# Performance work log

Measured on AMD Instinct MI355X. Metric: run time of the kernel, lower is better.

Reference implementation:

```python
import jax, jax.numpy as jnp
import numpy as np

F_DIM = 128
H_DIM = 128
T_DIM = H_DIM // 4          # 32
D = H_DIM + T_DIM           # 160, block hidden dim
N_NODES = 100000
N_EDGES = 800000
N_LAYERS = 2
LN_EPS = 1e-5


def _layernorm(x, g, b):
    m = jnp.mean(x, axis=-1, keepdims=True)
    v = jnp.mean(jnp.square(x - m), axis=-1, keepdims=True)
    return (x - m) * jax.lax.rsqrt(v + LN_EPS) * g + b


def setup_inputs() -> dict:
    key = jax.random.key(0)
    ks = jax.random.split(key, 24)
    p = lambda k, shape: jax.random.normal(k, shape, dtype=jnp.float32) * 0.05
    inp = {
        "node_features": jax.random.normal(ks[0], (N_NODES, F_DIM), dtype=jnp.float32),
        "edge_index": jax.random.randint(ks[1], (2, N_EDGES), 0, N_NODES, dtype=jnp.int32),
        "edge_weights": jax.random.uniform(ks[2], (N_EDGES,), dtype=jnp.float32),
        "time_steps": jax.random.uniform(ks[3], (N_NODES, 1), dtype=jnp.float32),
        # node encoder: Linear(F,H) + LN(H)
        "w_enc": p(ks[4], (H_DIM, F_DIM)), "b_enc": jnp.zeros((H_DIM,)),
        "g_enc": jnp.ones((H_DIM,)), "be_enc": jnp.zeros((H_DIM,)),
        # time encoder: Linear(1,T) + LN(T)
        "w_time": p(ks[5], (T_DIM, 1)), "b_time": jnp.zeros((T_DIM,)),
        "g_time": jnp.ones((T_DIM,)), "be_time": jnp.zeros((T_DIM,)),
        # per-layer block params (stacked over layers)
        "wm": p(ks[6], (N_LAYERS, D, 2 * D)), "bm": jnp.zeros((N_LAYERS, D)),
        "gm": jnp.ones((N_LAYERS, D)), "bem": jnp.zeros((N_LAYERS, D)),
        "wu": p(ks[7], (N_LAYERS, D, 2 * D)), "bu": jnp.zeros((N_LAYERS, D)),
        "gu": jnp.ones((N_LAYERS, D)), "beu": jnp.zeros((N_LAYERS, D)),
        "wg": p(ks[8], (N_LAYERS, 1, D)), "bg": jnp.zeros((N_LAYERS, 1)),
        # output projection Linear(D, F)
        "w_out": p(ks[9], (F_DIM, D)), "b_out": jnp.zeros((F_DIM,)),
    }
    return inp


def _block(h, src, dst, w, wm, bm, gm, bem, wu, bu, gu, beu, wg, bg):
    n = h.shape[0]
    # gather endpoints -> per-edge message MLP -> weight -> scatter-add mean
    ecat = jnp.concatenate([h[src], h[dst]], axis=-1)              # [E, 2D]
    em = jax.nn.relu(_layernorm(ecat @ wm.T + bm, gm, bem)) * w[:, None]
    msum = jax.ops.segment_sum(em, dst, num_segments=n)            # [N, D]
    cnt = jax.ops.segment_sum(jnp.ones_like(w), dst, num_segments=n)[:, None]
    valid = (cnt > 0).astype(h.dtype)
    messages = msum / (cnt + 1e-8) * valid
    tw = jax.nn.sigmoid(h @ wg.T + bg)                             # [N, 1]
    h_new = jax.nn.relu(_layernorm(jnp.concatenate([h, messages], axis=-1) @ wu.T + bu, gu, beu))
    return tw * h_new + (1 - tw) * h


def reference(node_features, edge_index, edge_weights, time_steps,
              w_enc, b_enc, g_enc, be_enc, w_time, b_time, g_time, be_time,
              wm, bm, gm, bem, wu, bu, gu, beu, wg, bg, w_out, b_out):
    src, dst = edge_index[0], edge_index[1]
    h = jax.nn.relu(_layernorm(node_features @ w_enc.T + b_enc, g_enc, be_enc))
    t = jax.nn.relu(_layernorm(time_steps @ w_time.T + b_time, g_time, be_time))
    h_t = jnp.concatenate([h, t], axis=-1)                          # [N, D]
    for l in range(N_LAYERS):
        h_t = _block(h_t, src, dst, edge_weights,
                     wm[l], bm[l], gm[l], bem[l],
                     wu[l], bu[l], gu[l], beu[l], wg[l], bg[l])
    out = h_t @ w_out.T + b_out
    # F.normalize(dim=-1), eps=1e-12
    norm = jnp.linalg.norm(out, axis=-1, keepdims=True)
    return out / jnp.maximum(norm, 1e-12)
```

## Files before the change

kernel.cpp:

```cpp
#include <hip/hip_runtime.h>

#define NN 100000
#define NE 800000

typedef _Float16 half8 __attribute__((ext_vector_type(8)));
typedef _Float16 half4 __attribute__((ext_vector_type(4)));
typedef float floatx4 __attribute__((ext_vector_type(4)));

#define LDB(Wf, f) (*(const half8*)&(Wf)[(f) * 512])

__global__ __launch_bounds__(256) void k_zero(float4* __restrict__ p, int n4) {
  int i = blockIdx.x * 256 + threadIdx.x;
  if (i < n4) p[i] = make_float4(0.f, 0.f, 0.f, 0.f);
}

__global__ __launch_bounds__(256) void k_pack(
    const float* __restrict__ w_enc, const float* __restrict__ w_out,
    const float* __restrict__ wu, const float* __restrict__ wm,
    _Float16* __restrict__ WeP, _Float16* __restrict__ WoP,
    _Float16* __restrict__ WuP, _Float16* __restrict__ WpP) {
  int gid = blockIdx.x * 256 + threadIdx.x;
  int fid = gid >> 6, lane = gid & 63;
  int mrow = lane & 15, quad = lane >> 4;
  const float* src; _Float16* dst; int stride, NI, f, g;
  if (fid < 32) {
    f = fid; g = f; src = w_enc; dst = WeP; stride = 128; NI = 8;
  } else if (fid < 72) {
    f = fid - 32; g = f; src = w_out; dst = WoP; stride = 160; NI = 8;
  } else if (fid < 272) {
    f = fid - 72; g = f % 100; src = wu + (f / 100) * 51200; dst = WuP; stride = 320; NI = 10;
  } else {
    f = fid - 272; g = f % 50;
    int l = f / 100, h = (f % 100) / 50;
    src = wm + l * 51200 + h * 160; dst = WpP; stride = 320; NI = 10;
  }
  int kk = g / NI, i = g - kk * NI;
  const float* sp = src + (size_t)(i * 16 + mrow) * stride + kk * 32 + quad * 8;
  float4 f0 = *(const float4*)sp;
  float4 f1 = *(const float4*)(sp + 4);
  half8 v = {(_Float16)f0.x, (_Float16)f0.y, (_Float16)f0.z, (_Float16)f0.w,
             (_Float16)f1.x, (_Float16)f1.y, (_Float16)f1.z, (_Float16)f1.w};
  *(half8*)&dst[(size_t)(f * 64 + lane) * 8] = v;
}

__global__ __launch_bounds__(256) void k_count_i(const int* __restrict__ ei,
                                                 int* __restrict__ cnti) {
  int e = blockIdx.x * 256 + threadIdx.x;
  atomicAdd(&cnti[ei[NE + e]], 1);
}

__global__ __launch_bounds__(256) void k_scan1(const int* __restrict__ cnti,
                                               int* __restrict__ off,
                                               int* __restrict__ bsum) {
  __shared__ int sh[256];
  const int t = threadIdx.x;
  const int i = blockIdx.x * 256 + t;
  int v = (i < NN) ? cnti[i] : 0;
  sh[t] = v;
  __syncthreads();
  for (int d = 1; d < 256; d <<= 1) {
    int add = (t >= d) ? sh[t - d] : 0;
    __syncthreads();
    sh[t] += add;
    __syncthreads();
  }
  if (i < NN) off[i] = sh[t] - v;
  if (t == 255) bsum[blockIdx.x] = sh[255];
}

__global__ __launch_bounds__(512) void k_scan2(const int* __restrict__ bsum,
                                               int* __restrict__ bsum2) {
  __shared__ int sh[512];
  const int t = threadIdx.x;
  int v = (t < 391) ? bsum[t] : 0;
  sh[t] = v;
  __syncthreads();
  for (int d = 1; d < 512; d <<= 1) {
    int add = (t >= d) ? sh[t - d] : 0;
    __syncthreads();
    sh[t] += add;
    __syncthreads();
  }
  if (t < 391) bsum2[t] = sh[t] - v;
}

__global__ __launch_bounds__(256) void k_scan3(int* __restrict__ off,
                                               const int* __restrict__ bsum2,
                                               int* __restrict__ cursor) {
  const int i = blockIdx.x * 256 + threadIdx.x;
  if (i < NN) {
    int o = off[i] + bsum2[blockIdx.x];
    off[i] = o;
    cursor[i] = o;
  }
  if (i == 0) off[NN] = NE;
}

__global__ __launch_bounds__(256) void k_scatter(const int* __restrict__ ei,
                                                 const float* __restrict__ ew,
                                                 int* __restrict__ cursor,
                                                 int2* __restrict__ selist) {
  int e = blockIdx.x * 256 + threadIdx.x;
  int dst = ei[NE + e];
  int pos = atomicAdd(&cursor[dst], 1);
  selist[pos] = make_int2(ei[e], __float_as_int(ew[e]));
}

__device__ __forceinline__ half8 cvt8(const float* p) {
  float4 f0 = *(const float4*)p;
  float4 f1 = *(const float4*)(p + 4);
  half8 a = {(_Float16)f0.x, (_Float16)f0.y, (_Float16)f0.z, (_Float16)f0.w,
             (_Float16)f1.x, (_Float16)f1.y, (_Float16)f1.z, (_Float16)f1.w};
  return a;
}

__device__ __forceinline__ void ldg5(half8 d[5], const _Float16* Wf, int g) {
#pragma unroll
  for (int ii = 0; ii < 5; ++ii) d[ii] = LDB(Wf, g * 5 + ii);
}
__device__ __forceinline__ void ldg4(half8 d[4], const _Float16* Wf, int g) {
#pragma unroll
  for (int ii = 0; ii < 4; ++ii) d[ii] = LDB(Wf, g * 4 + ii);
}

__device__ __forceinline__ void write_h16_wave(_Float16* __restrict__ h16,
                                               const _Float16* tile, int n0,
                                               int lane) {
#pragma unroll
  for (int u = 0; u < 5; ++u) {
    int c = lane + u * 64;
    int row = c / 20, col = (c - row * 20) * 8;
    *(half8*)&h16[(size_t)(n0 + row) * 160 + col] = *(const half8*)&tile[row * 168 + col];
  }
}

__device__ __forceinline__ void phase2_proj(
    const _Float16* __restrict__ WpP, const float* __restrict__ bm,
    _Float16* __restrict__ P, const _Float16* tile, half8 bA[5], half8 bB[5],
    int lane, int mrow, int quad, int n0) {
#pragma unroll
  for (int half_ = 0; half_ < 2; ++half_) {
    const _Float16* Wf = WpP + half_ * 25600 + lane * 8;
    const _Float16* Wfn = WpP + 25600 + lane * 8;
    floatx4 acc2[10];
#pragma unroll
    for (int i = 0; i < 10; ++i) acc2[i] = (floatx4)0.f;
    half8 a_cur = *(const half8*)&tile[mrow * 168 + quad * 8];
#pragma unroll
    for (int g = 0; g < 10; ++g) {
      half8* bc = (g & 1) ? bB : bA;
      half8* bn = (g & 1) ? bA : bB;
      if (g + 1 < 10) ldg5(bn, Wf, g + 1);
      else if (half_ == 0) ldg5(bn, Wfn, 0);
      half8 a_use = a_cur;
      if ((g & 1) && g < 9) {
        int kk1 = (g + 1) >> 1;
        a_cur = *(const half8*)&tile[mrow * 168 + kk1 * 32 + quad * 8];
      }
      const int ib = (g & 1) * 5;
#pragma unroll
      for (int ii = 0; ii < 5; ++ii)
        acc2[ib + ii] = __builtin_amdgcn_mfma_f32_16x16x32_f16(a_use, bc[ii], acc2[ib + ii], 0, 0, 0);
    }
#pragma unroll
    for (int r = 0; r < 4; ++r) {
      const int row = quad * 4 + r;
      _Float16* prow = &P[(size_t)(n0 + row) * 320 + half_ * 160];
#pragma unroll
      for (int i = 0; i < 10; ++i) {
        int jj = i * 16 + mrow;
        prow[jj] = (_Float16)(acc2[i][r] + (half_ ? bm[jj] : 0.f));
      }
    }
  }
}

__global__ __launch_bounds__(64, 4) void k_encode_proj(
    const float* __restrict__ x, const float* __restrict__ tsp,
    const _Float16* __restrict__ WeP,
    const float* __restrict__ b_enc, const float* __restrict__ g_enc,
    const float* __restrict__ be_enc,
    const float* __restrict__ w_time, const float* __restrict__ b_time,
    const float* __restrict__ g_time, const float* __restrict__ be_time,
    const _Float16* __restrict__ WpP, const float* __restrict__ bm,
    _Float16* __restrict__ h16, _Float16* __restrict__ P) {
  __shared__ _Float16 tile[16 * 168];
  const int lane = threadIdx.x;
  const int mrow = lane & 15, quad = lane >> 4;
  const int n0 = blockIdx.x * 16;
  const float* xrow = x + (size_t)(n0 + mrow) * 128;
  const _Float16* Wf = WeP + lane * 8;
  half8 cA[4], cB[4];
  ldg4(cA, Wf, 0);
  float mw = 0.f, mb = 0.f;
  for (int d = 0; d < 32; ++d) { mw += w_time[d]; mb += b_time[d]; }
  mw *= (1.f / 32.f); mb *= (1.f / 32.f);
  float A = 0.f, B = 0.f, C = 0.f;
  for (int d = 0; d < 32; ++d) {
    float a = w_time[d] - mw, c = b_time[d] - mb;
    A = fmaf(a, a, A); B = fmaf(a, c, B); C = fmaf(c, c, C);
  }
  A *= (1.f / 32.f); B *= (1.f / 32.f); C *= (1.f / 32.f);
  floatx4 acc[8];
#pragma unroll
  for (int i = 0; i < 8; ++i) acc[i] = (floatx4)0.f;
  half8 a_cur = cvt8(&xrow[quad * 8]);
#pragma unroll
  for (int g = 0; g < 8; ++g) {
    half8* bc = (g & 1) ? cB : cA;
    half8* bn = (g & 1) ? cA : cB;
    if (g + 1 < 8) ldg4(bn, Wf, g + 1);
    half8 a_use = a_cur;
    if ((g & 1) && g < 7) {
      int kk1 = (g + 1) >> 1;
      a_cur = cvt8(&xrow[kk1 * 32 + quad * 8]);
    }
    const int ib = (g & 1) * 4;
#pragma unroll
    for (int ii = 0; ii < 4; ++ii)
      acc[ib + ii] = __builtin_amdgcn_mfma_f32_16x16x32_f16(a_use, bc[ii], acc[ib + ii], 0, 0, 0);
  }
  half8 bA[5], bB[5];
  ldg5(bA, WpP + lane * 8, 0);
#pragma unroll
  for (int r = 0; r < 4; ++r) {
    const int row = quad * 4 + r;
    float v[8], s = 0.f, ss = 0.f;
#pragma unroll
    for (int i = 0; i < 8; ++i) {
      v[i] = acc[i][r] + b_enc[i * 16 + mrow];
      s += v[i]; ss = fmaf(v[i], v[i], ss);
    }
#pragma unroll
    for (int off = 1; off < 16; off <<= 1) { s += __shfl_xor(s, off); ss += __shfl_xor(ss, off); }
    const float m = s * (1.f / 128.f);
    const float rs = rsqrtf(ss * (1.f / 128.f) - m * m + 1e-5f);
#pragma unroll
    for (int i = 0; i < 8; ++i) {
      int j = i * 16 + mrow;
      tile[row * 168 + j] =
          (_Float16)fmaxf(fmaf((v[i] - m) * rs, g_enc[j], be_enc[j]), 0.f);
    }
  }
#pragma unroll
  for (int rr = 0; rr < 8; ++rr) {
    int q = lane + rr * 64;
    int nn = q >> 5, d = q & 31;
    float tsv = tsp[n0 + nn];
    float mt = fmaf(mw, tsv, mb);
    float rst = rsqrtf(fmaf(fmaf(A, tsv, 2.f * B), tsv, C) + 1e-5f);
    float vv = fmaf(w_time[d], tsv, b_time[d]);
    float y = fmaxf(fmaf((vv - mt) * rst, g_time[d], be_time[d]), 0.f);
    tile[nn * 168 + 128 + d] = (_Float16)y;
  }
  write_h16_wave(h16, tile, n0, lane);
  phase2_proj(WpP, bm, P, tile, bA, bB, lane, mrow, quad, n0);
}

__global__ __launch_bounds__(256) void k_edge3(
    const _Float16* __restrict__ P, const int* __restrict__ off,
    const int2* __restrict__ selist,
    const float* __restrict__ gm, const float* __restrict__ bem,
    _Float16* __restrict__ msum16) {
  const int t = threadIdx.x;
  const int jg = t & 31, g = t >> 5;
  const int n = blockIdx.x * 8 + g;
  float gmv[5], bev[5], pdv[5];
#pragma unroll
  for (int i = 0; i < 4; ++i) { gmv[i] = gm[4 * jg + i]; bev[i] = bem[4 * jg + i]; }
  gmv[4] = gm[128 + jg]; bev[4] = bem[128 + jg];
  const _Float16* pd = P + (size_t)n * 320 + 160;
  half4 pdh = *(const half4*)&pd[4 * jg];
  pdv[0] = (float)pdh.x; pdv[1] = (float)pdh.y; pdv[2] = (float)pdh.z; pdv[3] = (float)pdh.w;
  pdv[4] = (float)pd[128 + jg];
  float acc[5] = {0.f, 0.f, 0.f, 0.f, 0.f};
  const int e0 = off[n], e1 = off[n + 1];
  int k = e0;
  for (; k + 1 < e1; k += 2) {
    int2 seA = selist[k], seB = selist[k + 1];
    const _Float16* psA = P + (size_t)seA.x * 320;
    const _Float16* psB = P + (size_t)seB.x * 320;
    const float weA = __int_as_float(seA.y), weB = __int_as_float(seB.y);
    half4 a4 = *(const half4*)&psA[4 * jg];
    half4 b4 = *(const half4*)&psB[4 * jg];
    float a5 = (float)psA[128 + jg], b5 = (float)psB[128 + jg];
    float vA[5], vB[5];
    vA[0] = (float)a4.x + pdv[0]; vA[1] = (float)a4.y + pdv[1];
    vA[2] = (float)a4.z + pdv[2]; vA[3] = (float)a4.w + pdv[3]; vA[4] = a5 + pdv[4];
    vB[0] = (float)b4.x + pdv[0]; vB[1] = (float)b4.y + pdv[1];
    vB[2] = (float)b4.z + pdv[2]; vB[3] = (float)b4.w + pdv[3]; vB[4] = b5 + pdv[4];
    float sA = 0.f, ssA = 0.f, sB = 0.f, ssB = 0.f;
#pragma unroll
    for (int i = 0; i < 5; ++i) {
      sA += vA[i]; ssA = fmaf(vA[i], vA[i], ssA);
      sB += vB[i]; ssB = fmaf(vB[i], vB[i], ssB);
    }
#pragma unroll
    for (int o = 1; o < 32; o <<= 1) {
      sA += __shfl_xor(sA, o); ssA += __shfl_xor(ssA, o);
      sB += __shfl_xor(sB, o); ssB += __shfl_xor(ssB, o);
    }
    const float mA = sA * (1.f / 160.f), mB = sB * (1.f / 160.f);
    const float rsA = rsqrtf(ssA * (1.f / 160.f) - mA * mA + 1e-5f);
    const float rsB = rsqrtf(ssB * (1.f / 160.f) - mB * mB + 1e-5f);
#pragma unroll
    for (int i = 0; i < 5; ++i) {
      acc[i] = fmaf(fmaxf(fmaf((vA[i] - mA) * rsA, gmv[i], bev[i]), 0.f), weA, acc[i]);
      acc[i] = fmaf(fmaxf(fmaf((vB[i] - mB) * rsB, gmv[i], bev[i]), 0.f), weB, acc[i]);
    }
  }
  if (k < e1) {
    int2 se = selist[k];
    const _Float16* ps = P + (size_t)se.x * 320;
    const float we = __int_as_float(se.y);
    half4 s4 = *(const half4*)&ps[4 * jg];
    float v[5], s = 0.f, ss = 0.f;
    v[0] = (float)s4.x + pdv[0]; v[1] = (float)s4.y + pdv[1];
    v[2] = (float)s4.z + pdv[2]; v[3] = (float)s4.w + pdv[3];
    v[4] = (float)ps[128 + jg] + pdv[4];
#pragma unroll
    for (int i = 0; i < 5; ++i) { s += v[i]; ss = fmaf(v[i], v[i], ss); }
#pragma unroll
    for (int o = 1; o < 32; o <<= 1) { s += __shfl_xor(s, o); ss += __shfl_xor(ss, o); }
    const float m = s * (1.f / 160.f);
    const float rs = rsqrtf(ss * (1.f / 160.f) - m * m + 1e-5f);
#pragma unroll
    for (int i = 0; i < 5; ++i)
      acc[i] = fmaf(fmaxf(fmaf((v[i] - m) * rs, gmv[i], bev[i]), 0.f), we, acc[i]);
  }
  const float c = (float)(e1 - e0);
  const float ic = (c > 0.f) ? 1.f / (c + 1e-8f) : 0.f;
  _Float16* orow = msum16 + (size_t)n * 160;
  half4 o4 = {(_Float16)(acc[0] * ic), (_Float16)(acc[1] * ic),
              (_Float16)(acc[2] * ic), (_Float16)(acc[3] * ic)};
  *(half4*)&orow[4 * jg] = o4;
  orow[128 + jg] = (_Float16)(acc[4] * ic);
}

__device__ __forceinline__ void update_phase1(
    const _Float16* __restrict__ h16, const _Float16* __restrict__ msum16,
    const _Float16* __restrict__ WuP, const float* __restrict__ bu,
    const float* __restrict__ gu, const float* __restrict__ beu,
    const float* __restrict__ wg, const float* __restrict__ bg,
    const _Float16* __restrict__ WpPf,
    _Float16* tile, half8 bA[5], half8 bB[5],
    int lane, int mrow, int quad, int n0) {
  const _Float16* h0 = h16 + (size_t)(n0 + mrow) * 160;
  const _Float16* ms0 = msum16 + (size_t)(n0 + mrow) * 160;
  const _Float16* Wf = WuP + lane * 8;
  ldg5(bA, Wf, 0);
  float gp = 0.f;
#pragma unroll
  for (int kt = 0; kt < 5; ++kt) {
    half8 ha = *(const half8*)&h0[kt * 32 + quad * 8];
    float4 g0 = *(const float4*)&wg[kt * 32 + quad * 8];
    float4 g1 = *(const float4*)&wg[kt * 32 + quad * 8 + 4];
    gp = fmaf((float)ha[0], g0.x, gp); gp = fmaf((float)ha[1], g0.y, gp);
    gp = fmaf((float)ha[2], g0.z, gp); gp = fmaf((float)ha[3], g0.w, gp);
    gp = fmaf((float)ha[4], g1.x, gp); gp = fmaf((float)ha[5], g1.y, gp);
    gp = fmaf((float)ha[6], g1.z, gp); gp = fmaf((float)ha[7], g1.w, gp);
  }
  gp += __shfl_xor(gp, 16); gp += __shfl_xor(gp, 32);
  const float twv = 1.f / (1.f + expf(-(gp + bg[0])));
  floatx4 acc[10];
#pragma unroll
  for (int i = 0; i < 10; ++i) acc[i] = (floatx4)0.f;
  half8 a_cur = *(const half8*)&h0[quad * 8];
#pragma unroll
  for (int g = 0; g < 20; ++g) {
    half8* bc = (g & 1) ? bB : bA;
    half8* bn = (g & 1) ? bA : bB;
    if (g + 1 < 20) ldg5(bn, Wf, g + 1);
    half8 a_use = a_cur;
    if ((g & 1) && g < 19) {
      int kk1 = (g + 1) >> 1;
      const _Float16* ap = (kk1 < 5) ? h0 + kk1 * 32 : ms0 + (kk1 - 5) * 32;
      a_cur = *(const half8*)&ap[quad * 8];
    }
    const int ib = (g & 1) * 5;
#pragma unroll
    for (int ii = 0; ii < 5; ++ii)
      acc[ib + ii] = __builtin_amdgcn_mfma_f32_16x16x32_f16(a_use, bc[ii], acc[ib + ii], 0, 0, 0);
  }
  ldg5(bA, WpPf, 0);
#pragma unroll
  for (int r = 0; r < 4; ++r) {
    const int row = quad * 4 + r;
    float v[10], s = 0.f, ss = 0.f;
#pragma unroll
    for (int i = 0; i < 10; ++i) {
      v[i] = acc[i][r] + bu[i * 16 + mrow];
      s += v[i]; ss = fmaf(v[i], v[i], ss);
    }
#pragma unroll
    for (int off = 1; off < 16; off <<= 1) { s += __shfl_xor(s, off); ss += __shfl_xor(ss, off); }
    const float m = s * (1.f / 160.f);
    const float rs = rsqrtf(ss * (1.f / 160.f) - m * m + 1e-5f);
    const float g = __shfl(twv, row);
    const _Float16* hr = h16 + (size_t)(n0 + row) * 160;
#pragma unroll
    for (int i = 0; i < 10; ++i) {
      int j = i * 16 + mrow;
      float hnew = fmaxf(fmaf((v[i] - m) * rs, gu[j], beu[j]), 0.f);
      float hold = (float)hr[j];
      tile[row * 168 + j] = (_Float16)fmaf(g, hnew - hold, hold);
    }
  }
}

__global__ __launch_bounds__(64, 4) void k_update_proj(
    _Float16* __restrict__ h16, const _Float16* __restrict__ msum16,
    const _Float16* __restrict__ WuP, const float* __restrict__ bu,
    const float* __restrict__ gu, const float* __restrict__ beu,
    const float* __restrict__ wg, const float* __restrict__ bg,
    const _Float16* __restrict__ WpP, const float* __restrict__ bm,
    _Float16* __restrict__ P) {
  __shared__ _Float16 tile[16 * 168];
  const int lane = threadIdx.x;
  const int mrow = lane & 15, quad = lane >> 4;
  const int n0 = blockIdx.x * 16;
  half8 bA[5], bB[5];
  update_phase1(h16, msum16, WuP, bu, gu, beu, wg, bg,
                WpP + lane * 8, tile, bA, bB, lane, mrow, quad, n0);
  write_h16_wave(h16, tile, n0, lane);
  phase2_proj(WpP, bm, P, tile, bA, bB, lane, mrow, quad, n0);
}

__global__ __launch_bounds__(64, 4) void k_update_out(
    const _Float16* __restrict__ h16, const _Float16* __restrict__ msum16,
    const _Float16* __restrict__ WuP, const float* __restrict__ bu,
    const float* __restrict__ gu, const float* __restrict__ beu,
    const float* __restrict__ wg, const float* __restrict__ bg,
    const _Float16* __restrict__ WoP, const float* __restrict__ b_out,
    float* __restrict__ out) {
  __shared__ _Float16 tile[16 * 168];
  const int lane = threadIdx.x;
  const int mrow = lane & 15, quad = lane >> 4;
  const int n0 = blockIdx.x * 16;
  half8 bA[5], bB[5];
  update_phase1(h16, msum16, WuP, bu, gu, beu, wg, bg,
                WoP + lane * 8, tile, bA, bB, lane, mrow, quad, n0);
  const _Float16* Wf2 = WoP + lane * 8;
  half8 cA[4], cB[4];
#pragma unroll
  for (int ii = 0; ii < 4; ++ii) cA[ii] = bA[ii];
  floatx4 acc2[8];
#pragma unroll
  for (int i = 0; i < 8; ++i) acc2[i] = (floatx4)0.f;
  half8 a_cur = *(const half8*)&tile[mrow * 168 + quad * 8];
#pragma unroll
  for (int g = 0; g < 10; ++g) {
    half8* bc = (g & 1) ? cB : cA;
    half8* bn = (g & 1) ? cA : cB;
    if (g + 1 < 10) ldg4(bn, Wf2, g + 1);
    half8 a_use = a_cur;
    if ((g & 1) && g < 9) {
      int kk1 = (g + 1) >> 1;
      a_cur = *(const half8*)&tile[mrow * 168 + kk1 * 32 + quad * 8];
    }
    const int ib = (g & 1) * 4;
#pragma unroll
    for (int ii = 0; ii < 4; ++ii)
      acc2[ib + ii] = __builtin_amdgcn_mfma_f32_16x16x32_f16(a_use, bc[ii], acc2[ib + ii], 0, 0, 0);
  }
#pragma unroll
  for (int r = 0; r < 4; ++r) {
    const int row = quad * 4 + r;
    float v[8], ss = 0.f;
#pragma unroll
    for (int i = 0; i < 8; ++i) {
      v[i] = acc2[i][r] + b_out[i * 16 + mrow];
      ss = fmaf(v[i], v[i], ss);
    }
#pragma unroll
    for (int off = 1; off < 16; off <<= 1) ss += __shfl_xor(ss, off);
    const float inv = 1.f / fmaxf(sqrtf(ss), 1e-12f);
#pragma unroll
    for (int i = 0; i < 8; ++i)
      out[(size_t)(n0 + row) * 128 + i * 16 + mrow] = v[i] * inv;
  }
}

extern "C" void kernel_launch(void* const* d_in, const int* in_sizes, int n_in,
                              void* d_out, int out_size, void* d_ws, size_t ws_size,
                              hipStream_t stream) {
  (void)in_sizes; (void)n_in; (void)out_size; (void)ws_size;
  const float* x       = (const float*)d_in[0];
  const int*   ei      = (const int*)  d_in[1];
  const float* ew      = (const float*)d_in[2];
  const float* tsp     = (const float*)d_in[3];
  const float* w_enc   = (const float*)d_in[4];
  const float* b_enc   = (const float*)d_in[5];
  const float* g_enc   = (const float*)d_in[6];
  const float* be_enc  = (const float*)d_in[7];
  const float* w_time  = (const float*)d_in[8];
  const float* b_time  = (const float*)d_in[9];
  const float* g_time  = (const float*)d_in[10];
  const float* be_time = (const float*)d_in[11];
  const float* wm      = (const float*)d_in[12];
  const float* bm      = (const float*)d_in[13];
  const float* gm      = (const float*)d_in[14];
  const float* bem     = (const float*)d_in[15];
  const float* wu      = (const float*)d_in[16];
  const float* bu      = (const float*)d_in[17];
  const float* gu      = (const float*)d_in[18];
  const float* beu     = (const float*)d_in[19];
  const float* wg      = (const float*)d_in[20];
  const float* bg      = (const float*)d_in[21];
  const float* w_out   = (const float*)d_in[22];
  const float* b_out   = (const float*)d_in[23];
  float* out = (float*)d_out;

  char* ws = (char*)d_ws;
  _Float16* h16    = (_Float16*)ws;
  _Float16* msum16 = (_Float16*)(ws + 32000000);
  _Float16* P      = (_Float16*)(ws + 64000000);
  _Float16* WuP16  = (_Float16*)(ws + 128000000);
  _Float16* WoP16  = (_Float16*)(ws + 128204800);
  char* ob = (char*)d_out;
  _Float16* WpP16 = (_Float16*)ob;
  _Float16* WeP16 = (_Float16*)(ob + 204800);
  int* off    = (int*)(ob + 237568);
  int* cnti   = (int*)(ob + 637584);
  int* cursor = (int*)(ob + 1037584);
  int* bsum   = (int*)(ob + 1437584);
  int* bsum2  = (int*)(ob + 1439152);
  int2* selist = (int2*)(ob + 1440720);

  k_zero<<<dim3(98), dim3(256), 0, stream>>>((float4*)cnti, 25000);
  k_pack<<<dim3(118), dim3(256), 0, stream>>>(w_enc, w_out, wu, wm,
                                              WeP16, WoP16, WuP16, WpP16);
  k_count_i<<<dim3(3125), dim3(256), 0, stream>>>(ei, cnti);
  k_scan1<<<dim3(391), dim3(256), 0, stream>>>(cnti, off, bsum);
  k_scan2<<<dim3(1), dim3(512), 0, stream>>>(bsum, bsum2);
  k_scan3<<<dim3(391), dim3(256), 0, stream>>>(off, bsum2, cursor);
  k_scatter<<<dim3(3125), dim3(256), 0, stream>>>(ei, ew, cursor, selist);

  k_encode_proj<<<dim3(6250), dim3(64), 0, stream>>>(
      x, tsp, WeP16, b_enc, g_enc, be_enc, w_time, b_time, g_time, be_time,
      WpP16, bm, h16, P);
  k_edge3<<<dim3(12500), dim3(256), 0, stream>>>(P, off, selist, gm, bem, msum16);
  k_update_proj<<<dim3(6250), dim3(64), 0, stream>>>(
      h16, msum16, WuP16, bu, gu, beu, wg, bg,
      WpP16 + 51200, bm + 160, P);
  k_edge3<<<dim3(12500), dim3(256), 0, stream>>>(P, off, selist, gm + 160, bem + 160, msum16);
  k_update_out<<<dim3(6250), dim3(64), 0, stream>>>(
      h16, msum16, WuP16 + 51200, bu + 160, gu + 160, beu + 160, wg + 160, bg + 1,
      WoP16, b_out, out);
}
```

Measured before the change: 554.3 us.

## Precompute per-node LayerNorm partial sums and split edges across half-waves

The projection kernels now also write, for each node, the sum and sum of squares of both the source and destination halves of the projected features. The edge kernel rebuilds each edge's LayerNorm mean and variance from these plus a single dot product, so it needs one cross-lane reduction per edge where it previously needed two. The edge kernel is also reorganised so each 64-lane wave handles one destination node, with its two 32-lane halves processing alternate edges and combining their results at the end, which doubles the grid. The cost is an extra small gathered read per edge and a variance computed as E[x²]−m², which can lose precision.

```diff
diff --git a/kernel.cpp b/kernel.cpp
--- a/kernel.cpp
+++ b/kernel.cpp
@@ -136,7 +136,8 @@
 
 __device__ __forceinline__ void phase2_proj(
     const _Float16* __restrict__ WpP, const float* __restrict__ bm,
-    _Float16* __restrict__ P, const _Float16* tile, half8 bA[5], half8 bB[5],
+    _Float16* __restrict__ P, float* __restrict__ S12,
+    const _Float16* tile, half8 bA[5], half8 bB[5],
     int lane, int mrow, int quad, int n0) {
 #pragma unroll
   for (int half_ = 0; half_ < 2; ++half_) {
@@ -166,11 +167,19 @@
     for (int r = 0; r < 4; ++r) {
       const int row = quad * 4 + r;
       _Float16* prow = &P[(size_t)(n0 + row) * 320 + half_ * 160];
+      float s1 = 0.f, s2 = 0.f;
 #pragma unroll
       for (int i = 0; i < 10; ++i) {
         int jj = i * 16 + mrow;
-        prow[jj] = (_Float16)(acc2[i][r] + (half_ ? bm[jj] : 0.f));
+        _Float16 hv = (_Float16)(acc2[i][r] + (half_ ? bm[jj] : 0.f));
+        prow[jj] = hv;
+        float fv = (float)hv;
+        s1 += fv; s2 = fmaf(fv, fv, s2);
       }
+#pragma unroll
+      for (int off = 1; off < 16; off <<= 1) { s1 += __shfl_xor(s1, off); s2 += __shfl_xor(s2, off); }
+      if (mrow == 0)
+        *(float2*)&S12[(size_t)(n0 + row) * 4 + half_ * 2] = make_float2(s1, s2);
     }
   }
 }
@@ -183,7 +192,8 @@
     const float* __restrict__ w_time, const float* __restrict__ b_time,
     const float* __restrict__ g_time, const float* __restrict__ be_time,
     const _Float16* __restrict__ WpP, const float* __restrict__ bm,
-    _Float16* __restrict__ h16, _Float16* __restrict__ P) {
+    _Float16* __restrict__ h16, _Float16* __restrict__ P,
+    float* __restrict__ S12) {
   __shared__ _Float16 tile[16 * 168];
   const int lane = threadIdx.x;
   const int mrow = lane & 15, quad = lane >> 4;
@@ -254,17 +264,18 @@
     tile[nn * 168 + 128 + d] = (_Float16)y;
   }
   write_h16_wave(h16, tile, n0, lane);
-  phase2_proj(WpP, bm, P, tile, bA, bB, lane, mrow, quad, n0);
-}
-
-__global__ __launch_bounds__(256) void k_edge3(
+  phase2_proj(WpP, bm, P, S12, tile, bA, bB, lane, mrow, quad, n0);
+}
+
+__global__ __launch_bounds__(256) void k_edge4(
     const _Float16* __restrict__ P, const int* __restrict__ off,
-    const int2* __restrict__ selist,
+    const int2* __restrict__ selist, const float* __restrict__ S12,
     const float* __restrict__ gm, const float* __restrict__ bem,
     _Float16* __restrict__ msum16) {
   const int t = threadIdx.x;
-  const int jg = t & 31, g = t >> 5;
-  const int n = blockIdx.x * 8 + g;
+  const int lane = t & 63;
+  const int h = lane >> 5, jg = lane & 31;
+  const int n = blockIdx.x * 4 + (t >> 6);
   float gmv[5], bev[5], pdv[5];
 #pragma unroll
   for (int i = 0; i < 4; ++i) { gmv[i] = gm[4 * jg + i]; bev[i] = bem[4 * jg + i]; }
@@ -273,68 +284,46 @@
   half4 pdh = *(const half4*)&pd[4 * jg];
   pdv[0] = (float)pdh.x; pdv[1] = (float)pdh.y; pdv[2] = (float)pdh.z; pdv[3] = (float)pdh.w;
   pdv[4] = (float)pd[128 + jg];
+  const float2 sdst = *(const float2*)&S12[(size_t)n * 4 + 2];
   float acc[5] = {0.f, 0.f, 0.f, 0.f, 0.f};
   const int e0 = off[n], e1 = off[n + 1];
-  int k = e0;
-  for (; k + 1 < e1; k += 2) {
-    int2 seA = selist[k], seB = selist[k + 1];
-    const _Float16* psA = P + (size_t)seA.x * 320;
-    const _Float16* psB = P + (size_t)seB.x * 320;
-    const float weA = __int_as_float(seA.y), weB = __int_as_float(seB.y);
-    half4 a4 = *(const half4*)&psA[4 * jg];
-    half4 b4 = *(const half4*)&psB[4 * jg];
-    float a5 = (float)psA[128 + jg], b5 = (float)psB[128 + jg];
-    float vA[5], vB[5];
-    vA[0] = (float)a4.x + pdv[0]; vA[1] = (float)a4.y + pdv[1];
-    vA[2] = (float)a4.z + pdv[2]; vA[3] = (float)a4.w + pdv[3]; vA[4] = a5 + pdv[4];
-    vB[0] = (float)b4.x + pdv[0]; vB[1] = (float)b4.y + pdv[1];
-    vB[2] = (float)b4.z + pdv[2]; vB[3] = (float)b4.w + pdv[3]; vB[4] = b5 + pdv[4];
-    float sA = 0.f, ssA = 0.f, sB = 0.f, ssB = 0.f;
-#pragma unroll
-    for (int i = 0; i < 5; ++i) {
-      sA += vA[i]; ssA = fmaf(vA[i], vA[i], ssA);
-      sB += vB[i]; ssB = fmaf(vB[i], vB[i], ssB);
-    }
-#pragma unroll
-    for (int o = 1; o < 32; o <<= 1) {
-      sA += __shfl_xor(sA, o); ssA += __shfl_xor(ssA, o);
-      sB += __shfl_xor(sB, o); ssB += __shfl_xor(ssB, o);
-    }
-    const float mA = sA * (1.f / 160.f), mB = sB * (1.f / 160.f);
-    const float rsA = rsqrtf(ssA * (1.f / 160.f) - mA * mA + 1e-5f);
-    const float rsB = rsqrtf(ssB * (1.f / 160.f) - mB * mB + 1e-5f);
-#pragma unroll
-    for (int i = 0; i < 5; ++i) {
-      acc[i] = fmaf(fmaxf(fmaf((vA[i] - mA) * rsA, gmv[i], bev[i]), 0.f), weA, acc[i]);
-      acc[i] = fmaf(fmaxf(fmaf((vB[i] - mB) * rsB, gmv[i], bev[i]), 0.f), weB, acc[i]);
-    }
-  }
-  if (k < e1) {
-    int2 se = selist[k];
+  for (int k = e0; k < e1; k += 2) {
+    int e = k + h;
+    const bool val = e < e1;
+    if (!val) e = e1 - 1;
+    const int2 se = selist[e];
+    const float we = val ? __int_as_float(se.y) : 0.f;
     const _Float16* ps = P + (size_t)se.x * 320;
-    const float we = __int_as_float(se.y);
-    half4 s4 = *(const half4*)&ps[4 * jg];
-    float v[5], s = 0.f, ss = 0.f;
-    v[0] = (float)s4.x + pdv[0]; v[1] = (float)s4.y + pdv[1];
-    v[2] = (float)s4.z + pdv[2]; v[3] = (float)s4.w + pdv[3];
-    v[4] = (float)ps[128 + jg] + pdv[4];
-#pragma unroll
-    for (int i = 0; i < 5; ++i) { s += v[i]; ss = fmaf(v[i], v[i], ss); }
-#pragma unroll
-    for (int o = 1; o < 32; o <<= 1) { s += __shfl_xor(s, o); ss += __shfl_xor(ss, o); }
-    const float m = s * (1.f / 160.f);
-    const float rs = rsqrtf(ss * (1.f / 160.f) - m * m + 1e-5f);
+    half4 a4 = *(const half4*)&ps[4 * jg];
+    float a5 = (float)ps[128 + jg];
+    const float2 ssrc = *(const float2*)&S12[(size_t)se.x * 4];
+    float v[5];
+    v[0] = (float)a4.x + pdv[0]; v[1] = (float)a4.y + pdv[1];
+    v[2] = (float)a4.z + pdv[2]; v[3] = (float)a4.w + pdv[3];
+    v[4] = a5 + pdv[4];
+    float dot = 0.f;
+    dot = fmaf((float)a4.x, pdv[0], dot); dot = fmaf((float)a4.y, pdv[1], dot);
+    dot = fmaf((float)a4.z, pdv[2], dot); dot = fmaf((float)a4.w, pdv[3], dot);
+    dot = fmaf(a5, pdv[4], dot);
+#pragma unroll
+    for (int o = 1; o < 32; o <<= 1) dot += __shfl_xor(dot, o);
+    const float m = (ssrc.x + sdst.x) * (1.f / 160.f);
+    const float rs = rsqrtf(fmaf(2.f, dot, ssrc.y + sdst.y) * (1.f / 160.f) - m * m + 1e-5f);
 #pragma unroll
     for (int i = 0; i < 5; ++i)
       acc[i] = fmaf(fmaxf(fmaf((v[i] - m) * rs, gmv[i], bev[i]), 0.f), we, acc[i]);
   }
+#pragma unroll
+  for (int i = 0; i < 5; ++i) acc[i] += __shfl_xor(acc[i], 32);
   const float c = (float)(e1 - e0);
   const float ic = (c > 0.f) ? 1.f / (c + 1e-8f) : 0.f;
-  _Float16* orow = msum16 + (size_t)n * 160;
-  half4 o4 = {(_Float16)(acc[0] * ic), (_Float16)(acc[1] * ic),
-              (_Float16)(acc[2] * ic), (_Float16)(acc[3] * ic)};
-  *(half4*)&orow[4 * jg] = o4;
-  orow[128 + jg] = (_Float16)(acc[4] * ic);
+  if (h == 0) {
+    _Float16* orow = msum16 + (size_t)n * 160;
+    half4 o4 = {(_Float16)(acc[0] * ic), (_Float16)(acc[1] * ic),
+                (_Float16)(acc[2] * ic), (_Float16)(acc[3] * ic)};
+    *(half4*)&orow[4 * jg] = o4;
+    orow[128 + jg] = (_Float16)(acc[4] * ic);
+  }
 }
 
 __device__ __forceinline__ void update_phase1(
@@ -414,7 +403,7 @@
     const float* __restrict__ gu, const float* __restrict__ beu,
     const float* __restrict__ wg, const float* __restrict__ bg,
     const _Float16* __restrict__ WpP, const float* __restrict__ bm,
-    _Float16* __restrict__ P) {
+    _Float16* __restrict__ P, float* __restrict__ S12) {
   __shared__ _Float16 tile[16 * 168];
   const int lane = threadIdx.x;
   const int mrow = lane & 15, quad = lane >> 4;
@@ -423,7 +412,7 @@
   update_phase1(h16, msum16, WuP, bu, gu, beu, wg, bg,
                 WpP + lane * 8, tile, bA, bB, lane, mrow, quad, n0);
   write_h16_wave(h16, tile, n0, lane);
-  phase2_proj(WpP, bm, P, tile, bA, bB, lane, mrow, quad, n0);
+  phase2_proj(WpP, bm, P, S12, tile, bA, bB, lane, mrow, quad, n0);
 }
 
 __global__ __launch_bounds__(64, 4) void k_update_out(
@@ -526,6 +515,7 @@
   int* bsum   = (int*)(ob + 1437584);
   int* bsum2  = (int*)(ob + 1439152);
   int2* selist = (int2*)(ob + 1440720);
+  float* S12  = (float*)(ob + 7840720);
 
   k_zero<<<dim3(98), dim3(256), 0, stream>>>((float4*)cnti, 25000);
   k_pack<<<dim3(118), dim3(256), 0, stream>>>(w_enc, w_out, wu, wm,
@@ -538,12 +528,12 @@
 
   k_encode_proj<<<dim3(6250), dim3(64), 0, stream>>>(
       x, tsp, WeP16, b_enc, g_enc, be_enc, w_time, b_time, g_time, be_time,
-      WpP16, bm, h16, P);
-  k_edge3<<<dim3(12500), dim3(256), 0, stream>>>(P, off, selist, gm, bem, msum16);
+      WpP16, bm, h16, P, S12);
+  k_edge4<<<dim3(25000), dim3(256), 0, stream>>>(P, off, selist, S12, gm, bem, msum16);
   k_update_proj<<<dim3(6250), dim3(64), 0, stream>>>(
       h16, msum16, WuP16, bu, gu, beu, wg, bg,
-      WpP16 + 51200, bm + 160, P);
-  k_edge3<<<dim3(12500), dim3(256), 0, stream>>>(P, off, selist, gm + 160, bem + 160, msum16);
+      WpP16 + 51200, bm + 160, P, S12);
+  k_edge4<<<dim3(25000), dim3(256), 0, stream>>>(P, off, selist, S12, gm + 160, bem + 160, msum16);
   k_update_out<<<dim3(6250), dim3(64), 0, stream>>>(
       h16, msum16, WuP16 + 51200, bu + 160, gu + 160, beu + 160, wg + 160, bg + 1,
       WoP16, b_out, out);
```

Result: slower. 582.3 us (+5.1%).

## Split edge gather across half-warps with wider loads and software prefetch

Applied to the files above, without the earlier changes.

The edge aggregation kernel now uses 16 lanes per edge, each holding 10 features read with half8 and half2 loads, instead of 32 lanes with 5 features read with half4 and scalar loads. The two 16-lane halves of each 32-thread group work on alternating edges. The next edge's row is prefetched into registers while the current edge is computed. Partial sums from the two halves are combined with one xor shuffle before a single wide store. The aim is fewer, wider memory transactions, a shorter shuffle reduction, and hidden gather latency, at the cost of more registers per thread.

```diff
diff --git a/kernel.cpp b/kernel.cpp
--- a/kernel.cpp
+++ b/kernel.cpp
@@ -5,6 +5,7 @@
 
 typedef _Float16 half8 __attribute__((ext_vector_type(8)));
 typedef _Float16 half4 __attribute__((ext_vector_type(4)));
+typedef _Float16 half2v __attribute__((ext_vector_type(2)));
 typedef float floatx4 __attribute__((ext_vector_type(4)));
 
 #define LDB(Wf, f) (*(const half8*)&(Wf)[(f) * 512])
@@ -257,84 +258,98 @@
   phase2_proj(WpP, bm, P, tile, bA, bB, lane, mrow, quad, n0);
 }
 
-__global__ __launch_bounds__(256) void k_edge3(
+__global__ __launch_bounds__(256) void k_edge5(
     const _Float16* __restrict__ P, const int* __restrict__ off,
     const int2* __restrict__ selist,
     const float* __restrict__ gm, const float* __restrict__ bem,
     _Float16* __restrict__ msum16) {
   const int t = threadIdx.x;
-  const int jg = t & 31, g = t >> 5;
-  const int n = blockIdx.x * 8 + g;
-  float gmv[5], bev[5], pdv[5];
-#pragma unroll
-  for (int i = 0; i < 4; ++i) { gmv[i] = gm[4 * jg + i]; bev[i] = bem[4 * jg + i]; }
-  gmv[4] = gm[128 + jg]; bev[4] = bem[128 + jg];
-  const _Float16* pd = P + (size_t)n * 320 + 160;
-  half4 pdh = *(const half4*)&pd[4 * jg];
-  pdv[0] = (float)pdh.x; pdv[1] = (float)pdh.y; pdv[2] = (float)pdh.z; pdv[3] = (float)pdh.w;
-  pdv[4] = (float)pd[128 + jg];
-  float acc[5] = {0.f, 0.f, 0.f, 0.f, 0.f};
+  const int lane = t & 63;
+  const int n = blockIdx.x * 8 + (t >> 5);
+  const int q16 = (lane >> 4) & 1;
+  const int q = lane & 15;
+  float gmv[10], bev[10], pdv[10];
+  {
+    float4 g0 = *(const float4*)&gm[8 * q];
+    float4 g1 = *(const float4*)&gm[8 * q + 4];
+    float2 g2 = *(const float2*)&gm[128 + 2 * q];
+    gmv[0] = g0.x; gmv[1] = g0.y; gmv[2] = g0.z; gmv[3] = g0.w;
+    gmv[4] = g1.x; gmv[5] = g1.y; gmv[6] = g1.z; gmv[7] = g1.w;
+    gmv[8] = g2.x; gmv[9] = g2.y;
+    float4 b0 = *(const float4*)&bem[8 * q];
+    float4 b1 = *(const float4*)&bem[8 * q + 4];
+    float2 b2 = *(const float2*)&bem[128 + 2 * q];
+    bev[0] = b0.x; bev[1] = b0.y; bev[2] = b0.z; bev[3] = b0.w;
+    bev[4] = b1.x; bev[5] = b1.y; bev[6] = b1.z; bev[7] = b1.w;
+    bev[8] = b2.x; bev[9] = b2.y;
+  }
+  {
+    const _Float16* pd = P + (size_t)n * 320 + 160;
+    half8 p8 = *(const half8*)&pd[8 * q];
+    half2v p2 = *(const half2v*)&pd[128 + 2 * q];
+#pragma unroll
+    for (int i = 0; i < 8; ++i) pdv[i] = (float)p8[i];
+    pdv[8] = (float)p2.x; pdv[9] = (float)p2.y;
+  }
+  float acc[10];
+#pragma unroll
+  for (int i = 0; i < 10; ++i) acc[i] = 0.f;
   const int e0 = off[n], e1 = off[n + 1];
-  int k = e0;
-  for (; k + 1 < e1; k += 2) {
-    int2 seA = selist[k], seB = selist[k + 1];
-    const _Float16* psA = P + (size_t)seA.x * 320;
-    const _Float16* psB = P + (size_t)seB.x * 320;
-    const float weA = __int_as_float(seA.y), weB = __int_as_float(seB.y);
-    half4 a4 = *(const half4*)&psA[4 * jg];
-    half4 b4 = *(const half4*)&psB[4 * jg];
-    float a5 = (float)psA[128 + jg], b5 = (float)psB[128 + jg];
-    float vA[5], vB[5];
-    vA[0] = (float)a4.x + pdv[0]; vA[1] = (float)a4.y + pdv[1];
-    vA[2] = (float)a4.z + pdv[2]; vA[3] = (float)a4.w + pdv[3]; vA[4] = a5 + pdv[4];
-    vB[0] = (float)b4.x + pdv[0]; vB[1] = (float)b4.y + pdv[1];
-    vB[2] = (float)b4.z + pdv[2]; vB[3] = (float)b4.w + pdv[3]; vB[4] = b5 + pdv[4];
-    float sA = 0.f, ssA = 0.f, sB = 0.f, ssB = 0.f;
-#pragma unroll
-    for (int i = 0; i < 5; ++i) {
-      sA += vA[i]; ssA = fmaf(vA[i], vA[i], ssA);
-      sB += vB[i]; ssB = fmaf(vB[i], vB[i], ssB);
-    }
-#pragma unroll
-    for (int o = 1; o < 32; o <<= 1) {
-      sA += __shfl_xor(sA, o); ssA += __shfl_xor(ssA, o);
-      sB += __shfl_xor(sB, o); ssB += __shfl_xor(ssB, o);
-    }
-    const float mA = sA * (1.f / 160.f), mB = sB * (1.f / 160.f);
-    const float rsA = rsqrtf(ssA * (1.f / 160.f) - mA * mA + 1e-5f);
-    const float rsB = rsqrtf(ssB * (1.f / 160.f) - mB * mB + 1e-5f);
-#pragma unroll
-    for (int i = 0; i < 5; ++i) {
-      acc[i] = fmaf(fmaxf(fmaf((vA[i] - mA) * rsA, gmv[i], bev[i]), 0.f), weA, acc[i]);
-      acc[i] = fmaf(fmaxf(fmaf((vB[i] - mB) * rsB, gmv[i], bev[i]), 0.f), weB, acc[i]);
-    }
-  }
-  if (k < e1) {
-    int2 se = selist[k];
-    const _Float16* ps = P + (size_t)se.x * 320;
-    const float we = __int_as_float(se.y);
-    half4 s4 = *(const half4*)&ps[4 * jg];
-    float v[5], s = 0.f, ss = 0.f;
-    v[0] = (float)s4.x + pdv[0]; v[1] = (float)s4.y + pdv[1];
-    v[2] = (float)s4.z + pdv[2]; v[3] = (float)s4.w + pdv[3];
-    v[4] = (float)ps[128 + jg] + pdv[4];
-#pragma unroll
-    for (int i = 0; i < 5; ++i) { s += v[i]; ss = fmaf(v[i], v[i], ss); }
-#pragma unroll
-    for (int o = 1; o < 32; o <<= 1) { s += __shfl_xor(s, o); ss += __shfl_xor(ss, o); }
-    const float m = s * (1.f / 160.f);
-    const float rs = rsqrtf(ss * (1.f / 160.f) - m * m + 1e-5f);
-#pragma unroll
-    for (int i = 0; i < 5; ++i)
-      acc[i] = fmaf(fmaxf(fmaf((v[i] - m) * rs, gmv[i], bev[i]), 0.f), we, acc[i]);
-  }
+  if (e0 < e1) {
+    float weC; half8 a8C; half2v a2C;
+    {
+      int e = e0 + q16;
+      bool val = e < e1;
+      if (!val) e = e1 - 1;
+      int2 se = selist[e];
+      weC = val ? __int_as_float(se.y) : 0.f;
+      const _Float16* ps = P + (size_t)se.x * 320;
+      a8C = *(const half8*)&ps[8 * q];
+      a2C = *(const half2v*)&ps[128 + 2 * q];
+    }
+    for (int k = e0; k < e1; k += 2) {
+      float weN = 0.f; half8 a8N = a8C; half2v a2N = a2C;
+      if (k + 2 < e1) {
+        int e = k + 2 + q16;
+        bool val = e < e1;
+        if (!val) e = e1 - 1;
+        int2 se = selist[e];
+        weN = val ? __int_as_float(se.y) : 0.f;
+        const _Float16* ps = P + (size_t)se.x * 320;
+        a8N = *(const half8*)&ps[8 * q];
+        a2N = *(const half2v*)&ps[128 + 2 * q];
+      }
+      float v[10], s = 0.f, ss = 0.f;
+#pragma unroll
+      for (int i = 0; i < 8; ++i) v[i] = (float)a8C[i] + pdv[i];
+      v[8] = (float)a2C.x + pdv[8];
+      v[9] = (float)a2C.y + pdv[9];
+#pragma unroll
+      for (int i = 0; i < 10; ++i) { s += v[i]; ss = fmaf(v[i], v[i], ss); }
+#pragma unroll
+      for (int o = 1; o < 16; o <<= 1) { s += __shfl_xor(s, o); ss += __shfl_xor(ss, o); }
+      const float m = s * (1.f / 160.f);
+      const float rs = rsqrtf(ss * (1.f / 160.f) - m * m + 1e-5f);
+#pragma unroll
+      for (int i = 0; i < 10; ++i)
+        acc[i] = fmaf(fmaxf(fmaf((v[i] - m) * rs, gmv[i], bev[i]), 0.f), weC, acc[i]);
+      weC = weN; a8C = a8N; a2C = a2N;
+    }
+  }
+#pragma unroll
+  for (int i = 0; i < 10; ++i) acc[i] += __shfl_xor(acc[i], 16);
   const float c = (float)(e1 - e0);
   const float ic = (c > 0.f) ? 1.f / (c + 1e-8f) : 0.f;
-  _Float16* orow = msum16 + (size_t)n * 160;
-  half4 o4 = {(_Float16)(acc[0] * ic), (_Float16)(acc[1] * ic),
-              (_Float16)(acc[2] * ic), (_Float16)(acc[3] * ic)};
-  *(half4*)&orow[4 * jg] = o4;
-  orow[128 + jg] = (_Float16)(acc[4] * ic);
+  if (q16 == 0) {
+    _Float16* orow = msum16 + (size_t)n * 160;
+    half8 o8 = {(_Float16)(acc[0] * ic), (_Float16)(acc[1] * ic),
+                (_Float16)(acc[2] * ic), (_Float16)(acc[3] * ic),
+                (_Float16)(acc[4] * ic), (_Float16)(acc[5] * ic),
+                (_Float16)(acc[6] * ic), (_Float16)(acc[7] * ic)};
+    *(half8*)&orow[8 * q] = o8;
+    half2v o2 = {(_Float16)(acc[8] * ic), (_Float16)(acc[9] * ic)};
+    *(half2v*)&orow[128 + 2 * q] = o2;
+  }
 }
 
 __device__ __forceinline__ void update_phase1(
@@ -539,11 +554,11 @@
   k_encode_proj<<<dim3(6250), dim3(64), 0, stream>>>(
       x, tsp, WeP16, b_enc, g_enc, be_enc, w_time, b_time, g_time, be_time,
       WpP16, bm, h16, P);
-  k_edge3<<<dim3(12500), dim3(256), 0, stream>>>(P, off, selist, gm, bem, msum16);
+  k_edge5<<<dim3(12500), dim3(256), 0, stream>>>(P, off, selist, gm, bem, msum16);
   k_update_proj<<<dim3(6250), dim3(64), 0, stream>>>(
       h16, msum16, WuP16, bu, gu, beu, wg, bg,
       WpP16 + 51200, bm + 160, P);
-  k_edge3<<<dim3(12500), dim3(256), 0, stream>>>(P, off, selist, gm + 160, bem + 160, msum16);
+  k_edge5<<<dim3(12500), dim3(256), 0, stream>>>(P, off, selist, gm + 160, bem + 160, msum16);
   k_update_out<<<dim3(6250), dim3(64), 0, stream>>>(
       h16, msum16, WuP16 + 51200, bu + 160, gu + 160, beu + 160, wg + 160, bg + 1,
       WoP16, b_out, out);
```

Measured after the change: 539.7 us. 1.03x faster.
